# Kernel optimization log

Hardware: AMD Instinct MI355X
Metric: run time of the kernel (lower is better)

The kernel has to match this reference:

```python
import jax, jax.numpy as jnp
import numpy as np


def silu(x):
    return x * jax.nn.sigmoid(x)


def conv1x1(x, w, s, b, act):
    # x: [B,Ci,H,W], w: [Co,Ci]; BN folded into per-channel scale s / bias b
    y = jnp.einsum('oi,bihw->bohw', w, x) * s[None, :, None, None] + b[None, :, None, None]
    return silu(y) if act else y


def dwconv3x3(x, w, s, b):
    # depthwise 3x3, groups=C, padding SAME (autopad=1); w: [C,1,3,3]
    y = jax.lax.conv_general_dilated(
        x, w, window_strides=(1, 1), padding=[(1, 1), (1, 1)],
        dimension_numbers=('NCHW', 'OIHW', 'NCHW'),
        feature_group_count=x.shape[1])
    return y * s[None, :, None, None] + b[None, :, None, None]


def attention(x, qkv_w, qkv_s, qkv_b, pe_w, pe_s, pe_b, proj_w, proj_s, proj_b,
              num_heads=4, key_dim=32, head_dim=64):
    B, C, H, W = x.shape
    N = H * W
    scale = key_dim ** -0.5
    qkv = conv1x1(x, qkv_w, qkv_s, qkv_b, act=False)          # [B, C+2*nh*kd, H, W]
    qkv = qkv.reshape(B, num_heads, key_dim * 2 + head_dim, N)
    q = qkv[:, :, :key_dim]                                    # [B,nh,kd,N]
    k = qkv[:, :, key_dim:2 * key_dim]                         # [B,nh,kd,N]
    v = qkv[:, :, 2 * key_dim:]                                # [B,nh,hd,N]
    attn = jnp.einsum('bhdi,bhdj->bhij', q, k) * scale         # [B,nh,N,N]
    attn = jax.nn.softmax(attn, axis=-1)
    out = jnp.einsum('bhdj,bhij->bhdi', v, attn)               # [B,nh,hd,N]
    out = out.reshape(B, C, H, W) + dwconv3x3(v.reshape(B, C, H, W), pe_w, pe_s, pe_b)
    return conv1x1(out, proj_w, proj_s, proj_b, act=False)


def setup_inputs() -> dict:
    key = jax.random.key(0)
    ks = jax.random.split(key, 32)
    B, C1, H, W = 4, 512, 48, 48
    c = C1 // 2  # 256
    h = c + 2 * 32 * 4  # 512
    d = {'x': jax.random.normal(ks[0], (B, C1, H, W), jnp.float32)}
    def w(i, shape):
        return jax.random.normal(ks[i], shape, jnp.float32) * 0.05
    def s(i, n):
        return jax.random.uniform(ks[i], (n,), jnp.float32, 0.5, 1.5)
    def b(i, n):
        return jax.random.normal(ks[i], (n,), jnp.float32) * 0.05
    d['cv1_w'], d['cv1_s'], d['cv1_b'] = w(1, (2 * c, C1)), s(2, 2 * c), b(3, 2 * c)
    d['qkv_w'], d['qkv_s'], d['qkv_b'] = w(4, (h, c)), s(5, h), b(6, h)
    d['pe_w'], d['pe_s'], d['pe_b'] = w(7, (c, 1, 3, 3)), s(8, c), b(9, c)
    d['proj_w'], d['proj_s'], d['proj_b'] = w(10, (c, c)), s(11, c), b(12, c)
    d['ffn1_w'], d['ffn1_s'], d['ffn1_b'] = w(13, (2 * c, c)), s(14, 2 * c), b(15, 2 * c)
    d['ffn2_w'], d['ffn2_s'], d['ffn2_b'] = w(16, (c, 2 * c)), s(17, c), b(18, c)
    d['cv2_w'], d['cv2_s'], d['cv2_b'] = w(19, (C1, 2 * c)), s(20, C1), b(21, C1)
    return d


def reference(x, cv1_w, cv1_s, cv1_b, qkv_w, qkv_s, qkv_b, pe_w, pe_s, pe_b,
              proj_w, proj_s, proj_b, ffn1_w, ffn1_s, ffn1_b, ffn2_w, ffn2_s, ffn2_b,
              cv2_w, cv2_s, cv2_b):
    c = cv1_w.shape[0] // 2  # hidden channels (256)
    ab = conv1x1(x, cv1_w, cv1_s, cv1_b, act=True)
    a, bb = ab[:, :c], ab[:, c:]
    bb = bb + attention(bb, qkv_w, qkv_s, qkv_b, pe_w, pe_s, pe_b,
                        proj_w, proj_s, proj_b)
    f = conv1x1(bb, ffn1_w, ffn1_s, ffn1_b, act=True)
    bb = bb + conv1x1(f, ffn2_w, ffn2_s, ffn2_b, act=False)
    return conv1x1(jnp.concatenate([a, bb], axis=1), cv2_w, cv2_s, cv2_b, act=True)
```

## Files before the change

kernel.cpp:

```cpp
#include <hip/hip_runtime.h>
#include <math.h>

#define N_SP 2304
#define HW 48

typedef unsigned short u16;
typedef short s8v  __attribute__((ext_vector_type(8)));
typedef short s4v  __attribute__((ext_vector_type(4)));
typedef u16   u16x8 __attribute__((ext_vector_type(8)));
typedef float f32x4 __attribute__((ext_vector_type(4)));
typedef unsigned u32x4 __attribute__((ext_vector_type(4)));

__device__ __forceinline__ short f2bf(float x) {
    unsigned u = __float_as_uint(x);
    u += 0x7FFFu + ((u >> 16) & 1u);
    return (short)(u >> 16);
}
__device__ __forceinline__ float bf2f(u16 u) {
    return __uint_as_float((unsigned)u << 16);
}
__device__ __forceinline__ float fexp2(float x) { return __builtin_amdgcn_exp2f(x); }
__device__ __forceinline__ float frcp(float x)  { return __builtin_amdgcn_rcpf(x); }
__device__ __forceinline__ float fsilu(float v) {
    return v * frcp(1.f + fexp2(-1.4426950408889634f * v));
}
__device__ __forceinline__ unsigned cvtpk(float lo, float hi) {
    unsigned r;
    asm("v_cvt_pk_bf16_f32 %0, %1, %2" : "=v"(r) : "v"(lo), "v"(hi));
    return r;
}
__device__ __forceinline__ void gload16(const void* g, void* l) {
    __builtin_amdgcn_global_load_lds(
        (const __attribute__((address_space(1))) void*)g,
        (__attribute__((address_space(3))) void*)l, 16, 0, 0);
}
__device__ __forceinline__ void bar_lgkm() {
    asm volatile("s_waitcnt lgkmcnt(0)" ::: "memory");
    __builtin_amdgcn_s_barrier();
}

__global__ __launch_bounds__(256) void cvt_w(
    const float* __restrict__ s0, const float* __restrict__ s1,
    const float* __restrict__ s2, const float* __restrict__ s3,
    const float* __restrict__ s4, const float* __restrict__ s5,
    u16* __restrict__ d0, u16* __restrict__ d1, u16* __restrict__ d2,
    u16* __restrict__ d3, u16* __restrict__ d4, u16* __restrict__ d5)
{
    int id = blockIdx.x * 256 + threadIdx.x;
    const int c0 = 65536, c1 = c0 + 32768, c2 = c1 + 16384,
              c3 = c2 + 32768, c4 = c3 + 32768, c5 = c4 + 65536;
    if (id >= c5) return;
    const float* s; u16* d; int off;
    if      (id < c0) { s = s0; d = d0; off = id; }
    else if (id < c1) { s = s1; d = d1; off = id - c0; }
    else if (id < c2) { s = s2; d = d2; off = id - c1; }
    else if (id < c3) { s = s3; d = d3; off = id - c2; }
    else if (id < c4) { s = s4; d = d4; off = id - c3; }
    else              { s = s5; d = d5; off = id - c4; }
    float4 v = ((const float4*)s)[off];
    s4v p; p[0] = f2bf(v.x); p[1] = f2bf(v.y); p[2] = f2bf(v.z); p[3] = f2bf(v.w);
    ((s4v*)d)[off] = p;
}

__global__ __launch_bounds__(256) void transpose_x(const float* __restrict__ X,
                                                   u16* __restrict__ XT)
{
    __shared__ float tile[64][65];
    const int n0 = blockIdx.x * 64, c0 = blockIdx.y * 64, b = blockIdx.z;
    const float* src = X + (long)b * 512 * N_SP;
    u16* dst = XT + (long)b * N_SP * 512;
    const int t = threadIdx.x;
    #pragma unroll
    for (int it = 0; it < 16; ++it) {
        int id = t + 256 * it;
        int cl = id >> 6, nl = id & 63;
        tile[cl][nl] = src[(long)(c0 + cl) * N_SP + n0 + nl];
    }
    __syncthreads();
    #pragma unroll
    for (int it = 0; it < 16; ++it) {
        int id = t + 256 * it;
        int nl = id >> 6, cl = id & 63;
        dst[(long)(n0 + nl) * 512 + c0 + cl] = f2bf(tile[cl][nl]);
    }
}

template <int OMODE>
__global__ __launch_bounds__(256) void mfma_gemm(
    const u16* __restrict__ A1, const u16* __restrict__ A2, int K1,
    int sA1, int sA2, int K,
    const u16* __restrict__ W,
    const float* __restrict__ S, const float* __restrict__ Bi,
    const u16* __restrict__ Res, int sR,
    void* __restrict__ OutP, int sO, int Mtot,
    int act)
{
    __shared__ u16 Al[3][64][64];
    __shared__ u16 Bl[3][64][64];
    const int t  = threadIdx.x;
    const int n0 = blockIdx.x * 64;
    const int o0 = blockIdx.y * 64;
    const int lane = t & 63, w = t >> 6;
    const int wn = (w & 1) * 32, wo = (w >> 1) * 32;
    const int li = lane & 15, g = lane >> 4;

    const int b_blk = n0 / N_SP;
    const int n_in0 = n0 - b_blk * N_SP;

    f32x4 acc[2][2];
    #pragma unroll
    for (int fm = 0; fm < 2; ++fm)
        #pragma unroll
        for (int fn = 0; fn < 2; ++fn) acc[fm][fn] = f32x4{0.f, 0.f, 0.f, 0.f};

    auto issue = [&](int buf, int k0) {
        #pragma unroll
        for (int q = 0; q < 2; ++q) {
            int c = t + q * 256;
            int row = c >> 3;
            int col = ((c & 7) ^ (row & 7)) * 8;
            int kk = k0 + col;
            const u16* ga = (kk < K1) ? (A1 + (long)(n0 + row) * sA1 + kk)
                                      : (A2 + (long)(n0 + row) * sA2 + (kk - K1));
            gload16(ga, (u16*)Al[buf] + (q * 256 + w * 64) * 8);
            gload16(W + (long)(o0 + row) * K + k0 + col,
                    (u16*)Bl[buf] + (q * 256 + w * 64) * 8);
        }
    };

    const int NK = K >> 6;
    issue(0, 0);
    if (NK > 1) issue(1, 64);

    for (int ks = 0; ks < NK; ++ks) {
        if (ks + 1 < NK) asm volatile("s_waitcnt vmcnt(4)" ::: "memory");
        else             asm volatile("s_waitcnt vmcnt(0)" ::: "memory");
        __builtin_amdgcn_s_barrier();
        if (ks + 2 < NK) issue((ks + 2) % 3, (ks + 2) << 6);
        const int cur = ks % 3;
        #pragma unroll
        for (int k2 = 0; k2 < 2; ++k2) {
            s8v af[2], bfv[2];
            #pragma unroll
            for (int fm = 0; fm < 2; ++fm) {
                int row = wn + fm * 16 + li;
                af[fm] = *(const s8v*)&Al[cur][row][((g + 4 * k2) ^ (li & 7)) * 8];
            }
            #pragma unroll
            for (int fn = 0; fn < 2; ++fn) {
                int row = wo + fn * 16 + li;
                bfv[fn] = *(const s8v*)&Bl[cur][row][((g + 4 * k2) ^ (li & 7)) * 8];
            }
            #pragma unroll
            for (int fm = 0; fm < 2; ++fm)
                #pragma unroll
                for (int fn = 0; fn < 2; ++fn)
                    acc[fm][fn] = __builtin_amdgcn_mfma_f32_16x16x32_bf16(
                        af[fm], bfv[fn], acc[fm][fn], 0, 0, 0);
        }
    }

    #pragma unroll
    for (int fn = 0; fn < 2; ++fn) {
        const int o = o0 + wo + fn * 16 + li;
        const float sc2 = S[o], bi = Bi[o];
        #pragma unroll
        for (int fm = 0; fm < 2; ++fm) {
            const int nb  = n0 + wn + fm * 16 + 4 * g;
            const int nib = n_in0 + wn + fm * 16 + 4 * g;
            float y[4];
            #pragma unroll
            for (int r = 0; r < 4; ++r) {
                float v = acc[fm][fn][r] * sc2 + bi;
                if (act) v = fsilu(v);
                y[r] = v;
            }
            if (Res) {
                #pragma unroll
                for (int r = 0; r < 4; ++r)
                    y[r] += bf2f(Res[(long)(nb + r) * sR + o]);
            }
            if (OMODE == 0) {
                u16* O = (u16*)OutP;
                #pragma unroll
                for (int r = 0; r < 4; ++r)
                    O[(long)(nb + r) * sO + o] = (u16)f2bf(y[r]);
            } else if (OMODE == 1) {
                u16* O = (u16*)OutP + (long)b_blk * Mtot * N_SP + (long)o * N_SP + nib;
                s4v pk;
                #pragma unroll
                for (int r = 0; r < 4; ++r) pk[r] = f2bf(y[r]);
                *(s4v*)O = pk;
            } else {
                float* O = (float*)OutP + (long)b_blk * Mtot * N_SP + (long)o * N_SP + nib;
                *(float4*)O = make_float4(y[0], y[1], y[2], y[3]);
            }
        }
    }
}

__global__ __launch_bounds__(256) void attn_mfma(const u16* __restrict__ qkv,
    u16* __restrict__ Opart, float* __restrict__ mpart, float* __restrict__ lpart)
{
    const int N = N_SP;
    __shared__ u16 Klds[2][64][40];
    __shared__ u16 Vlds[2][64][72];

    const int i0 = blockIdx.x * 128;
    const int bh = blockIdx.y;
    const int z  = blockIdx.z;
    const int b = bh >> 2, h = bh & 3;
    const int t = threadIdx.x;
    const int w = t >> 6;
    const int lane = t & 63;
    const int li = lane & 15;
    const int g  = lane >> 4;
    const float qscale = 0.17677669529663687f * 1.4426950408889634f;

    const u16* qp = qkv + ((long)b * 512 + (long)h * 128) * N;
    const u16* kp = qp + 32L * N;
    const u16* vp = qp + 64L * N;

    const int ia = i0 + w * 16 + li;
    const int ib = ia + 64;

    s8v qf[2];
    #pragma unroll
    for (int r = 0; r < 8; ++r) {
        qf[0][r] = f2bf(bf2f(qp[(long)(8 * g + r) * N + ia]) * qscale);
        qf[1][r] = f2bf(bf2f(qp[(long)(8 * g + r) * N + ib]) * qscale);
    }

    f32x4 oacc[2][4];
    #pragma unroll
    for (int q = 0; q < 2; ++q)
        #pragma unroll
        for (int dt = 0; dt < 4; ++dt) oacc[q][dt] = f32x4{0.f, 0.f, 0.f, 0.f};
    float m_run[2] = {-1e30f, -1e30f}, l_run[2] = {0.f, 0.f};

    const int kj  = lane;
    const int kd0 = w * 8;
    const int vd  = t >> 2;
    const int vjb = (t & 3) * 16;

    const int jbase = z * 576;
    u16x8 kr, vr0, vr1;
    auto ldregs = [&](int j0) {
        const u16* kpp = kp + j0 + kj;
        #pragma unroll
        for (int u = 0; u < 8; ++u) kr[u] = kpp[(long)(kd0 + u) * N];
        vr0 = *(const u16x8*)(vp + (long)vd * N + j0 + vjb);
        vr1 = *(const u16x8*)(vp + (long)vd * N + j0 + vjb + 8);
    };

    ldregs(jbase);
    *(u16x8*)&Klds[0][kj][kd0]     = kr;
    *(u16x8*)&Vlds[0][vd][vjb]     = vr0;
    *(u16x8*)&Vlds[0][vd][vjb + 8] = vr1;
    ldregs(jbase + 64);
    bar_lgkm();

    int cur = 0;
    for (int it = 0; it < 9; ++it) {
        if (it + 1 < 9) {
            *(u16x8*)&Klds[cur ^ 1][kj][kd0]     = kr;
            *(u16x8*)&Vlds[cur ^ 1][vd][vjb]     = vr0;
            *(u16x8*)&Vlds[cur ^ 1][vd][vjb + 8] = vr1;
            if (it + 2 < 9) ldregs(jbase + (it + 2) * 64);
        }

        f32x4 sacc[2][4];
        #pragma unroll
        for (int js = 0; js < 4; ++js) {
            s8v kf = *(const s8v*)&Klds[cur][js * 16 + li][8 * g];
            f32x4 zz = f32x4{0.f, 0.f, 0.f, 0.f};
            sacc[0][js] = __builtin_amdgcn_mfma_f32_16x16x32_bf16(kf, qf[0], zz, 0, 0, 0);
            sacc[1][js] = __builtin_amdgcn_mfma_f32_16x16x32_bf16(kf, qf[1], zz, 0, 0, 0);
        }

        #pragma unroll
        for (int q = 0; q < 2; ++q) {
            float tm = -1e30f;
            #pragma unroll
            for (int js = 0; js < 4; ++js)
                #pragma unroll
                for (int r = 0; r < 4; ++r) tm = fmaxf(tm, sacc[q][js][r]);
            tm = fmaxf(tm, __shfl_xor(tm, 16, 64));
            tm = fmaxf(tm, __shfl_xor(tm, 32, 64));
            if (__any(tm > m_run[q] + 8.f)) {
                float mnew = fmaxf(m_run[q], tm);
                float scl  = fexp2(m_run[q] - mnew);
                l_run[q] *= scl;
                #pragma unroll
                for (int dt = 0; dt < 4; ++dt) oacc[q][dt] *= scl;
                m_run[q] = mnew;
            }
            float ts = 0.f;
            #pragma unroll
            for (int js = 0; js < 4; ++js)
                #pragma unroll
                for (int r = 0; r < 4; ++r) {
                    float p = fexp2(sacc[q][js][r] - m_run[q]);
                    sacc[q][js][r] = p;
                    ts += p;
                }
            ts += __shfl_xor(ts, 16, 64);
            ts += __shfl_xor(ts, 32, 64);
            l_run[q] += ts;
        }

        #pragma unroll
        for (int ks = 0; ks < 2; ++ks) {
            s8v pf[2];
            #pragma unroll
            for (int q = 0; q < 2; ++q) {
                u32x4 pw;
                pw[0] = cvtpk(sacc[q][2 * ks][0],     sacc[q][2 * ks][1]);
                pw[1] = cvtpk(sacc[q][2 * ks][2],     sacc[q][2 * ks][3]);
                pw[2] = cvtpk(sacc[q][2 * ks + 1][0], sacc[q][2 * ks + 1][1]);
                pw[3] = cvtpk(sacc[q][2 * ks + 1][2], sacc[q][2 * ks + 1][3]);
                pf[q] = __builtin_bit_cast(s8v, pw);
            }
            #pragma unroll
            for (int dt = 0; dt < 4; ++dt) {
                int d = dt * 16 + li;
                s4v lo = *(const s4v*)&Vlds[cur][d][32 * ks + 4 * g];
                s4v hi = *(const s4v*)&Vlds[cur][d][32 * ks + 16 + 4 * g];
                s8v vf = __builtin_shufflevector(lo, hi, 0, 1, 2, 3, 4, 5, 6, 7);
                oacc[0][dt] = __builtin_amdgcn_mfma_f32_16x16x32_bf16(vf, pf[0], oacc[0][dt], 0, 0, 0);
                oacc[1][dt] = __builtin_amdgcn_mfma_f32_16x16x32_bf16(vf, pf[1], oacc[1][dt], 0, 0, 0);
            }
        }

        if (it + 1 < 9) bar_lgkm();
        cur ^= 1;
    }

    const long cb = (long)(z * 16 + bh);
    #pragma unroll
    for (int q = 0; q < 2; ++q) {
        const int i = q ? ib : ia;
        #pragma unroll
        for (int dt = 0; dt < 4; ++dt)
            #pragma unroll
            for (int r = 0; r < 4; ++r)
                Opart[(cb * 64 + dt * 16 + 4 * g + r) * N + i] = (u16)f2bf(oacc[q][dt][r]);
        if (g == 0) {
            mpart[cb * N + i] = m_run[q];
            lpart[cb * N + i] = l_run[q];
        }
    }
}

__global__ __launch_bounds__(256) void attn_combine(
    const u16* __restrict__ Opart, const float* __restrict__ mpart,
    const float* __restrict__ lpart, const u16* __restrict__ qkv,
    const float* __restrict__ pw, const float* __restrict__ ps,
    const float* __restrict__ pb, u16* __restrict__ attnT)
{
    const int N = N_SP;
    const int i0 = blockIdx.x * 64;
    const int bh = blockIdx.y;
    const int b = bh >> 2, h = bh & 3;
    const int t = threadIdx.x;
    const int il = t & 63, dq = t >> 6;
    const int d0 = dq * 16;
    const int i = i0 + il;

    float mm[4], ll[4];
    #pragma unroll
    for (int c = 0; c < 4; ++c) {
        mm[c] = mpart[((long)(c * 16 + bh)) * N + i];
        ll[c] = lpart[((long)(c * 16 + bh)) * N + i];
    }
    float ms = fmaxf(fmaxf(mm[0], mm[1]), fmaxf(mm[2], mm[3]));
    float wc[4], lsum = 0.f;
    #pragma unroll
    for (int c = 0; c < 4; ++c) {
        wc[c] = fexp2(mm[c] - ms);
        lsum += wc[c] * ll[c];
    }
    float inv = frcp(lsum);

    const int y = i / HW, x = i - (i / HW) * HW;
    const int y0ok = (y > 0), y1ok = (y < HW - 1);
    const int x0ok = (x > 0), x1ok = (x < HW - 1);
    const u16* vbase = qkv + ((long)b * 512 + (long)h * 128 + 64) * N;

    u16 ob[16];
    #pragma unroll
    for (int dd = 0; dd < 16; ++dd) {
        const int d = d0 + dd;
        const int cg = h * 64 + d;
        float o = 0.f;
        #pragma unroll
        for (int c = 0; c < 4; ++c)
            o += wc[c] * bf2f(Opart[((long)(c * 16 + bh) * 64 + d) * N + i]);
        o *= inv;
        const u16* src = vbase + (long)d * N;
        const float* w9 = pw + cg * 9;
        float s = 0.f;
        #pragma unroll
        for (int dy = -1; dy <= 1; ++dy) {
            if ((dy < 0 && !y0ok) || (dy > 0 && !y1ok)) continue;
            const u16* row = src + (y + dy) * HW;
            if (x0ok) s += w9[(dy + 1) * 3 + 0] * bf2f(row[x - 1]);
            s += w9[(dy + 1) * 3 + 1] * bf2f(row[x]);
            if (x1ok) s += w9[(dy + 1) * 3 + 2] * bf2f(row[x + 1]);
        }
        o += s * ps[cg] + pb[cg];
        ob[dd] = (u16)f2bf(o);
    }
    u16* dst = attnT + ((long)b * N + i) * 256 + h * 64 + d0;
    *(u16x8*)dst       = *(u16x8*)&ob[0];
    *(u16x8*)(dst + 8) = *(u16x8*)&ob[8];
}

extern "C" void kernel_launch(void* const* d_in, const int* in_sizes, int n_in,
                              void* d_out, int out_size, void* d_ws, size_t ws_size,
                              hipStream_t stream)
{
    const long N = N_SP;
    const float* x      = (const float*)d_in[0];
    const float* cv1_w  = (const float*)d_in[1];
    const float* cv1_s  = (const float*)d_in[2];
    const float* cv1_b  = (const float*)d_in[3];
    const float* qkv_w  = (const float*)d_in[4];
    const float* qkv_s  = (const float*)d_in[5];
    const float* qkv_b  = (const float*)d_in[6];
    const float* pe_w   = (const float*)d_in[7];
    const float* pe_s   = (const float*)d_in[8];
    const float* pe_b   = (const float*)d_in[9];
    const float* proj_w = (const float*)d_in[10];
    const float* proj_s = (const float*)d_in[11];
    const float* proj_b = (const float*)d_in[12];
    const float* ffn1_w = (const float*)d_in[13];
    const float* ffn1_s = (const float*)d_in[14];
    const float* ffn1_b = (const float*)d_in[15];
    const float* ffn2_w = (const float*)d_in[16];
    const float* ffn2_s = (const float*)d_in[17];
    const float* ffn2_b = (const float*)d_in[18];
    const float* cv2_w  = (const float*)d_in[19];
    const float* cv2_s  = (const float*)d_in[20];
    const float* cv2_b  = (const float*)d_in[21];
    float* out = (float*)d_out;

    u16* ws = (u16*)d_ws;
    u16* xT      = ws;
    u16* abT     = xT      + 4L * N * 512;
    u16* qkvb    = abT     + 4L * N * 512;
    u16* attnT   = qkvb    + 4L * N * 512;
    u16* bb2T    = attnT   + 4L * N * 256;
    u16* fT      = bb2T    + 4L * N * 256;
    u16* bb3T    = fT      + 4L * N * 512;
    u16* w_cv1   = bb3T    + 4L * N * 256;
    u16* w_qkv   = w_cv1   + 512L * 512;
    u16* w_proj  = w_qkv   + 512L * 256;
    u16* w_ffn1  = w_proj  + 256L * 256;
    u16* w_ffn2  = w_ffn1  + 512L * 256;
    u16* w_cv2   = w_ffn2  + 256L * 512;
    u16* Opart   = w_cv2   + 512L * 512;
    float* mpart = (float*)(Opart + 4L * 16 * 64 * N);
    float* lpart = mpart + 4L * 16 * N;

    dim3 blk(256);
    const int BIGK = 1 << 28;

    cvt_w<<<960, blk, 0, stream>>>(cv1_w, qkv_w, proj_w, ffn1_w, ffn2_w, cv2_w,
                                   w_cv1, w_qkv, w_proj, w_ffn1, w_ffn2, w_cv2);
    transpose_x<<<dim3(36, 8, 4), blk, 0, stream>>>(x, xT);

    mfma_gemm<0><<<dim3(144, 8), blk, 0, stream>>>(
        xT, nullptr, BIGK, 512, 0, 512, w_cv1, cv1_s, cv1_b,
        nullptr, 0, abT, 512, 512, 1);

    mfma_gemm<1><<<dim3(144, 8), blk, 0, stream>>>(
        abT + 256, nullptr, BIGK, 512, 0, 256, w_qkv, qkv_s, qkv_b,
        nullptr, 0, qkvb, 0, 512, 0);

    attn_mfma<<<dim3(18, 16, 4), blk, 0, stream>>>(qkvb, Opart, mpart, lpart);

    attn_combine<<<dim3(36, 16), blk, 0, stream>>>(
        Opart, mpart, lpart, qkvb, pe_w, pe_s, pe_b, attnT);

    mfma_gemm<0><<<dim3(144, 4), blk, 0, stream>>>(
        attnT, nullptr, BIGK, 256, 0, 256, w_proj, proj_s, proj_b,
        abT + 256, 512, bb2T, 256, 256, 0);

    mfma_gemm<0><<<dim3(144, 8), blk, 0, stream>>>(
        bb2T, nullptr, BIGK, 256, 0, 256, w_ffn1, ffn1_s, ffn1_b,
        nullptr, 0, fT, 512, 512, 1);

    mfma_gemm<0><<<dim3(144, 4), blk, 0, stream>>>(
        fT, nullptr, BIGK, 512, 0, 512, w_ffn2, ffn2_s, ffn2_b,
        bb2T, 256, bb3T, 256, 256, 0);

    mfma_gemm<2><<<dim3(144, 8), blk, 0, stream>>>(
        abT, bb3T, 256, 512, 256, 512, w_cv2, cv2_s, cv2_b,
        nullptr, 0, out, 0, 512, 1);
}
```

Measured before the change: 148.8 us.

## Widen GEMM output tile to 128 with K-step 32 and halve attention KV splits

The GEMM kernel now computes 64x128 output tiles per block with a K step of 32 and a new 4-slot XOR swizzle, so each wave handles a 32x64 sub-tile with more MFMAs per A fragment load. The goal is more reuse of the activation tile per block and fewer blocks per GEMM. Separately, the split-K attention kernel drops from 4 to 2 key splits of 1152 keys each. That halves the Opart/mpart/lpart partial traffic and the combine work, but leaves half as many attention blocks to fill the GPU. Halving the block counts may hurt occupancy on a large CU count device.

Result: slower. 162.6 us (+9.3%).

```diff
diff --git a/kernel.cpp b/kernel.cpp
--- a/kernel.cpp
+++ b/kernel.cpp
@@ -95,73 +95,72 @@
     void* __restrict__ OutP, int sO, int Mtot,
     int act)
 {
-    __shared__ u16 Al[3][64][64];
-    __shared__ u16 Bl[3][64][64];
+    __shared__ u16 Al[3][64][32];
+    __shared__ u16 Bl[3][128][32];
     const int t  = threadIdx.x;
     const int n0 = blockIdx.x * 64;
-    const int o0 = blockIdx.y * 64;
+    const int o0 = blockIdx.y * 128;
     const int lane = t & 63, w = t >> 6;
-    const int wn = (w & 1) * 32, wo = (w >> 1) * 32;
+    const int wn = (w & 1) * 32, wo = (w >> 1) * 64;
     const int li = lane & 15, g = lane >> 4;
 
     const int b_blk = n0 / N_SP;
     const int n_in0 = n0 - b_blk * N_SP;
 
-    f32x4 acc[2][2];
+    f32x4 acc[2][4];
     #pragma unroll
     for (int fm = 0; fm < 2; ++fm)
         #pragma unroll
-        for (int fn = 0; fn < 2; ++fn) acc[fm][fn] = f32x4{0.f, 0.f, 0.f, 0.f};
+        for (int fn = 0; fn < 4; ++fn) acc[fm][fn] = f32x4{0.f, 0.f, 0.f, 0.f};
 
     auto issue = [&](int buf, int k0) {
-        #pragma unroll
-        for (int q = 0; q < 2; ++q) {
-            int c = t + q * 256;
-            int row = c >> 3;
-            int col = ((c & 7) ^ (row & 7)) * 8;
-            int kk = k0 + col;
+        {
+            int row = t >> 2, slot = t & 3;
+            int kk = k0 + ((slot ^ ((row >> 1) & 3)) << 3);
             const u16* ga = (kk < K1) ? (A1 + (long)(n0 + row) * sA1 + kk)
                                       : (A2 + (long)(n0 + row) * sA2 + (kk - K1));
-            gload16(ga, (u16*)Al[buf] + (q * 256 + w * 64) * 8);
-            gload16(W + (long)(o0 + row) * K + k0 + col,
-                    (u16*)Bl[buf] + (q * 256 + w * 64) * 8);
+            gload16(ga, (u16*)Al[buf] + t * 8);
+        }
+        #pragma unroll
+        for (int q = 0; q < 2; ++q) {
+            int idx = t + q * 256;
+            int row = idx >> 2, slot = idx & 3;
+            int kc = (slot ^ ((row >> 1) & 3)) << 3;
+            gload16(W + (long)(o0 + row) * K + k0 + kc, (u16*)Bl[buf] + idx * 8);
         }
     };
 
-    const int NK = K >> 6;
+    const int NK = K >> 5;
     issue(0, 0);
-    if (NK > 1) issue(1, 64);
+    if (NK > 1) issue(1, 32);
 
     for (int ks = 0; ks < NK; ++ks) {
-        if (ks + 1 < NK) asm volatile("s_waitcnt vmcnt(4)" ::: "memory");
+        if (ks + 1 < NK) asm volatile("s_waitcnt vmcnt(3)" ::: "memory");
         else             asm volatile("s_waitcnt vmcnt(0)" ::: "memory");
         __builtin_amdgcn_s_barrier();
-        if (ks + 2 < NK) issue((ks + 2) % 3, (ks + 2) << 6);
+        if (ks + 2 < NK) issue((ks + 2) % 3, (ks + 2) << 5);
         const int cur = ks % 3;
-        #pragma unroll
-        for (int k2 = 0; k2 < 2; ++k2) {
-            s8v af[2], bfv[2];
-            #pragma unroll
-            for (int fm = 0; fm < 2; ++fm) {
-                int row = wn + fm * 16 + li;
-                af[fm] = *(const s8v*)&Al[cur][row][((g + 4 * k2) ^ (li & 7)) * 8];
-            }
-            #pragma unroll
-            for (int fn = 0; fn < 2; ++fn) {
-                int row = wo + fn * 16 + li;
-                bfv[fn] = *(const s8v*)&Bl[cur][row][((g + 4 * k2) ^ (li & 7)) * 8];
-            }
-            #pragma unroll
-            for (int fm = 0; fm < 2; ++fm)
-                #pragma unroll
-                for (int fn = 0; fn < 2; ++fn)
-                    acc[fm][fn] = __builtin_amdgcn_mfma_f32_16x16x32_bf16(
-                        af[fm], bfv[fn], acc[fm][fn], 0, 0, 0);
-        }
-    }
-
-    #pragma unroll
-    for (int fn = 0; fn < 2; ++fn) {
+        s8v af[2], bfv[4];
+        #pragma unroll
+        for (int fm = 0; fm < 2; ++fm) {
+            int row = wn + fm * 16 + li;
+            af[fm] = *(const s8v*)&Al[cur][row][(g ^ ((row >> 1) & 3)) << 3];
+        }
+        #pragma unroll
+        for (int fn = 0; fn < 4; ++fn) {
+            int row = wo + fn * 16 + li;
+            bfv[fn] = *(const s8v*)&Bl[cur][row][(g ^ ((row >> 1) & 3)) << 3];
+        }
+        #pragma unroll
+        for (int fm = 0; fm < 2; ++fm)
+            #pragma unroll
+            for (int fn = 0; fn < 4; ++fn)
+                acc[fm][fn] = __builtin_amdgcn_mfma_f32_16x16x32_bf16(
+                    af[fm], bfv[fn], acc[fm][fn], 0, 0, 0);
+    }
+
+    #pragma unroll
+    for (int fn = 0; fn < 4; ++fn) {
         const int o = o0 + wo + fn * 16 + li;
         const float sc2 = S[o], bi = Bi[o];
         #pragma unroll
@@ -243,7 +242,8 @@
     const int vd  = t >> 2;
     const int vjb = (t & 3) * 16;
 
-    const int jbase = z * 576;
+    const int jbase = z * 1152;
+    const int NT = 18;
     u16x8 kr, vr0, vr1;
     auto ldregs = [&](int j0) {
         const u16* kpp = kp + j0 + kj;
@@ -261,12 +261,12 @@
     bar_lgkm();
 
     int cur = 0;
-    for (int it = 0; it < 9; ++it) {
-        if (it + 1 < 9) {
+    for (int it = 0; it < NT; ++it) {
+        if (it + 1 < NT) {
             *(u16x8*)&Klds[cur ^ 1][kj][kd0]     = kr;
             *(u16x8*)&Vlds[cur ^ 1][vd][vjb]     = vr0;
             *(u16x8*)&Vlds[cur ^ 1][vd][vjb + 8] = vr1;
-            if (it + 2 < 9) ldregs(jbase + (it + 2) * 64);
+            if (it + 2 < NT) ldregs(jbase + (it + 2) * 64);
         }
 
         f32x4 sacc[2][4];
@@ -332,7 +332,7 @@
             }
         }
 
-        if (it + 1 < 9) bar_lgkm();
+        if (it + 1 < NT) bar_lgkm();
         cur ^= 1;
     }
 
@@ -367,16 +367,16 @@
     const int d0 = dq * 16;
     const int i = i0 + il;
 
-    float mm[4], ll[4];
-    #pragma unroll
-    for (int c = 0; c < 4; ++c) {
+    float mm[2], ll[2];
+    #pragma unroll
+    for (int c = 0; c < 2; ++c) {
         mm[c] = mpart[((long)(c * 16 + bh)) * N + i];
         ll[c] = lpart[((long)(c * 16 + bh)) * N + i];
     }
-    float ms = fmaxf(fmaxf(mm[0], mm[1]), fmaxf(mm[2], mm[3]));
-    float wc[4], lsum = 0.f;
-    #pragma unroll
-    for (int c = 0; c < 4; ++c) {
+    float ms = fmaxf(mm[0], mm[1]);
+    float wc[2], lsum = 0.f;
+    #pragma unroll
+    for (int c = 0; c < 2; ++c) {
         wc[c] = fexp2(mm[c] - ms);
         lsum += wc[c] * ll[c];
     }
@@ -394,7 +394,7 @@
         const int cg = h * 64 + d;
         float o = 0.f;
         #pragma unroll
-        for (int c = 0; c < 4; ++c)
+        for (int c = 0; c < 2; ++c)
             o += wc[c] * bf2f(Opart[((long)(c * 16 + bh) * 64 + d) * N + i]);
         o *= inv;
         const u16* src = vbase + (long)d * N;
@@ -460,8 +460,8 @@
     u16* w_ffn2  = w_ffn1  + 512L * 256;
     u16* w_cv2   = w_ffn2  + 256L * 512;
     u16* Opart   = w_cv2   + 512L * 512;
-    float* mpart = (float*)(Opart + 4L * 16 * 64 * N);
-    float* lpart = mpart + 4L * 16 * N;
+    float* mpart = (float*)(Opart + 2L * 16 * 64 * N);
+    float* lpart = mpart + 2L * 16 * N;
 
     dim3 blk(256);
     const int BIGK = 1 << 28;
@@ -470,32 +470,32 @@
                                    w_cv1, w_qkv, w_proj, w_ffn1, w_ffn2, w_cv2);
     transpose_x<<<dim3(36, 8, 4), blk, 0, stream>>>(x, xT);
 
-    mfma_gemm<0><<<dim3(144, 8), blk, 0, stream>>>(
+    mfma_gemm<0><<<dim3(144, 4), blk, 0, stream>>>(
         xT, nullptr, BIGK, 512, 0, 512, w_cv1, cv1_s, cv1_b,
         nullptr, 0, abT, 512, 512, 1);
 
-    mfma_gemm<1><<<dim3(144, 8), blk, 0, stream>>>(
+    mfma_gemm<1><<<dim3(144, 4), blk, 0, stream>>>(
         abT + 256, nullptr, BIGK, 512, 0, 256, w_qkv, qkv_s, qkv_b,
         nullptr, 0, qkvb, 0, 512, 0);
 
-    attn_mfma<<<dim3(18, 16, 4), blk, 0, stream>>>(qkvb, Opart, mpart, lpart);
+    attn_mfma<<<dim3(18, 16, 2), blk, 0, stream>>>(qkvb, Opart, mpart, lpart);
 
     attn_combine<<<dim3(36, 16), blk, 0, stream>>>(
         Opart, mpart, lpart, qkvb, pe_w, pe_s, pe_b, attnT);
 
-    mfma_gemm<0><<<dim3(144, 4), blk, 0, stream>>>(
+    mfma_gemm<0><<<dim3(144, 2), blk, 0, stream>>>(
         attnT, nullptr, BIGK, 256, 0, 256, w_proj, proj_s, proj_b,
         abT + 256, 512, bb2T, 256, 256, 0);
 
-    mfma_gemm<0><<<dim3(144, 8), blk, 0, stream>>>(
+    mfma_gemm<0><<<dim3(144, 4), blk, 0, stream>>>(
         bb2T, nullptr, BIGK, 256, 0, 256, w_ffn1, ffn1_s, ffn1_b,
         nullptr, 0, fT, 512, 512, 1);
 
-    mfma_gemm<0><<<dim3(144, 4), blk, 0, stream>>>(
+    mfma_gemm<0><<<dim3(144, 2), blk, 0, stream>>>(
         fT, nullptr, BIGK, 512, 0, 512, w_ffn2, ffn2_s, ffn2_b,
         bb2T, 256, bb3T, 256, 256, 0);
 
-    mfma_gemm<2><<<dim3(144, 8), blk, 0, stream>>>(
+    mfma_gemm<2><<<dim3(144, 4), blk, 0, stream>>>(
         abT, bb3T, 256, 512, 256, 512, w_cv2, cv2_s, cv2_b,
         nullptr, 0, out, 0, 512, 1);
 }
```

## Remap block indices for XCD-local L2 reuse and merge prep kernels

Applied to the files above, without the earlier changes.

Flattens GEMM and attention grids to 1D and remaps block IDs so that blocks landing on the same XCD (block id mod 8) share the same spatial rows or batch-head slices. The aim is better L2 locality across the eight XCDs of the MI355X. It also fuses the weight conversion and input transpose kernels into one launch to save a kernel launch. The remap assumes round-robin XCD dispatch and grid sizes divisible by 8 and 18.

Measured after the change: 145.5 us. 1.02x faster.

```diff
diff --git a/kernel.cpp b/kernel.cpp
--- a/kernel.cpp
+++ b/kernel.cpp
@@ -39,37 +39,37 @@
     __builtin_amdgcn_s_barrier();
 }
 
-__global__ __launch_bounds__(256) void cvt_w(
+__global__ __launch_bounds__(256) void prep(
+    const float* __restrict__ X, u16* __restrict__ XT,
     const float* __restrict__ s0, const float* __restrict__ s1,
     const float* __restrict__ s2, const float* __restrict__ s3,
     const float* __restrict__ s4, const float* __restrict__ s5,
     u16* __restrict__ d0, u16* __restrict__ d1, u16* __restrict__ d2,
     u16* __restrict__ d3, u16* __restrict__ d4, u16* __restrict__ d5)
 {
-    int id = blockIdx.x * 256 + threadIdx.x;
-    const int c0 = 65536, c1 = c0 + 32768, c2 = c1 + 16384,
-              c3 = c2 + 32768, c4 = c3 + 32768, c5 = c4 + 65536;
-    if (id >= c5) return;
-    const float* s; u16* d; int off;
-    if      (id < c0) { s = s0; d = d0; off = id; }
-    else if (id < c1) { s = s1; d = d1; off = id - c0; }
-    else if (id < c2) { s = s2; d = d2; off = id - c1; }
-    else if (id < c3) { s = s3; d = d3; off = id - c2; }
-    else if (id < c4) { s = s4; d = d4; off = id - c3; }
-    else              { s = s5; d = d5; off = id - c4; }
-    float4 v = ((const float4*)s)[off];
-    s4v p; p[0] = f2bf(v.x); p[1] = f2bf(v.y); p[2] = f2bf(v.z); p[3] = f2bf(v.w);
-    ((s4v*)d)[off] = p;
-}
-
-__global__ __launch_bounds__(256) void transpose_x(const float* __restrict__ X,
-                                                   u16* __restrict__ XT)
-{
     __shared__ float tile[64][65];
-    const int n0 = blockIdx.x * 64, c0 = blockIdx.y * 64, b = blockIdx.z;
+    const int t = threadIdx.x;
+    if (blockIdx.x < 960) {
+        int id = blockIdx.x * 256 + t;
+        const int c0 = 65536, c1 = c0 + 32768, c2 = c1 + 16384,
+                  c3 = c2 + 32768, c4 = c3 + 32768, c5 = c4 + 65536;
+        if (id >= c5) return;
+        const float* s; u16* d; int off;
+        if      (id < c0) { s = s0; d = d0; off = id; }
+        else if (id < c1) { s = s1; d = d1; off = id - c0; }
+        else if (id < c2) { s = s2; d = d2; off = id - c1; }
+        else if (id < c3) { s = s3; d = d3; off = id - c2; }
+        else if (id < c4) { s = s4; d = d4; off = id - c3; }
+        else              { s = s5; d = d5; off = id - c4; }
+        float4 v = ((const float4*)s)[off];
+        s4v p; p[0] = f2bf(v.x); p[1] = f2bf(v.y); p[2] = f2bf(v.z); p[3] = f2bf(v.w);
+        ((s4v*)d)[off] = p;
+        return;
+    }
+    const int bid = blockIdx.x - 960;
+    const int n0 = (bid % 36) * 64, c0 = ((bid / 36) & 7) * 64, b = bid / 288;
     const float* src = X + (long)b * 512 * N_SP;
     u16* dst = XT + (long)b * N_SP * 512;
-    const int t = threadIdx.x;
     #pragma unroll
     for (int it = 0; it < 16; ++it) {
         int id = t + 256 * it;
@@ -85,7 +85,7 @@
     }
 }
 
-template <int OMODE>
+template <int NO, int OMODE>
 __global__ __launch_bounds__(256) void mfma_gemm(
     const u16* __restrict__ A1, const u16* __restrict__ A2, int K1,
     int sA1, int sA2, int K,
@@ -98,8 +98,10 @@
     __shared__ u16 Al[3][64][64];
     __shared__ u16 Bl[3][64][64];
     const int t  = threadIdx.x;
-    const int n0 = blockIdx.x * 64;
-    const int o0 = blockIdx.y * 64;
+    const int p = blockIdx.x;
+    const int cx = p & 7, q = p >> 3;
+    const int n0 = (cx * 18 + q / NO) * 64;
+    const int o0 = (q % NO) * 64;
     const int lane = t & 63, w = t >> 6;
     const int wn = (w & 1) * 32, wo = (w >> 1) * 32;
     const int li = lane & 15, g = lane >> 4;
@@ -115,16 +117,16 @@
 
     auto issue = [&](int buf, int k0) {
         #pragma unroll
-        for (int q = 0; q < 2; ++q) {
-            int c = t + q * 256;
+        for (int qq = 0; qq < 2; ++qq) {
+            int c = t + qq * 256;
             int row = c >> 3;
             int col = ((c & 7) ^ (row & 7)) * 8;
             int kk = k0 + col;
             const u16* ga = (kk < K1) ? (A1 + (long)(n0 + row) * sA1 + kk)
                                       : (A2 + (long)(n0 + row) * sA2 + (kk - K1));
-            gload16(ga, (u16*)Al[buf] + (q * 256 + w * 64) * 8);
+            gload16(ga, (u16*)Al[buf] + (qq * 256 + w * 64) * 8);
             gload16(W + (long)(o0 + row) * K + k0 + col,
-                    (u16*)Bl[buf] + (q * 256 + w * 64) * 8);
+                    (u16*)Bl[buf] + (qq * 256 + w * 64) * 8);
         }
     };
 
@@ -206,9 +208,11 @@
     __shared__ u16 Klds[2][64][40];
     __shared__ u16 Vlds[2][64][72];
 
-    const int i0 = blockIdx.x * 128;
-    const int bh = blockIdx.y;
-    const int z  = blockIdx.z;
+    const int p = blockIdx.x;
+    const int cx = p & 7, q = p >> 3;
+    const int i0 = (q % 18) * 128;
+    const int bhz = cx + 8 * (q / 18);
+    const int bh = bhz & 15, z = bhz >> 4;
     const int b = bh >> 2, h = bh & 3;
     const int t = threadIdx.x;
     const int w = t >> 6;
@@ -233,9 +237,9 @@
 
     f32x4 oacc[2][4];
     #pragma unroll
-    for (int q = 0; q < 2; ++q)
-        #pragma unroll
-        for (int dt = 0; dt < 4; ++dt) oacc[q][dt] = f32x4{0.f, 0.f, 0.f, 0.f};
+    for (int q2 = 0; q2 < 2; ++q2)
+        #pragma unroll
+        for (int dt = 0; dt < 4; ++dt) oacc[q2][dt] = f32x4{0.f, 0.f, 0.f, 0.f};
     float m_run[2] = {-1e30f, -1e30f}, l_run[2] = {0.f, 0.f};
 
     const int kj  = lane;
@@ -279,47 +283,47 @@
         }
 
         #pragma unroll
-        for (int q = 0; q < 2; ++q) {
+        for (int q2 = 0; q2 < 2; ++q2) {
             float tm = -1e30f;
             #pragma unroll
             for (int js = 0; js < 4; ++js)
                 #pragma unroll
-                for (int r = 0; r < 4; ++r) tm = fmaxf(tm, sacc[q][js][r]);
+                for (int r = 0; r < 4; ++r) tm = fmaxf(tm, sacc[q2][js][r]);
             tm = fmaxf(tm, __shfl_xor(tm, 16, 64));
             tm = fmaxf(tm, __shfl_xor(tm, 32, 64));
-            if (__any(tm > m_run[q] + 8.f)) {
-                float mnew = fmaxf(m_run[q], tm);
-                float scl  = fexp2(m_run[q] - mnew);
-                l_run[q] *= scl;
-                #pragma unroll
-                for (int dt = 0; dt < 4; ++dt) oacc[q][dt] *= scl;
-                m_run[q] = mnew;
+            if (__any(tm > m_run[q2] + 8.f)) {
+                float mnew = fmaxf(m_run[q2], tm);
+                float scl  = fexp2(m_run[q2] - mnew);
+                l_run[q2] *= scl;
+                #pragma unroll
+                for (int dt = 0; dt < 4; ++dt) oacc[q2][dt] *= scl;
+                m_run[q2] = mnew;
             }
             float ts = 0.f;
             #pragma unroll
             for (int js = 0; js < 4; ++js)
                 #pragma unroll
                 for (int r = 0; r < 4; ++r) {
-                    float p = fexp2(sacc[q][js][r] - m_run[q]);
-                    sacc[q][js][r] = p;
-                    ts += p;
+                    float pv = fexp2(sacc[q2][js][r] - m_run[q2]);
+                    sacc[q2][js][r] = pv;
+                    ts += pv;
                 }
             ts += __shfl_xor(ts, 16, 64);
             ts += __shfl_xor(ts, 32, 64);
-            l_run[q] += ts;
+            l_run[q2] += ts;
         }
 
         #pragma unroll
         for (int ks = 0; ks < 2; ++ks) {
             s8v pf[2];
             #pragma unroll
-            for (int q = 0; q < 2; ++q) {
+            for (int q2 = 0; q2 < 2; ++q2) {
                 u32x4 pw;
-                pw[0] = cvtpk(sacc[q][2 * ks][0],     sacc[q][2 * ks][1]);
-                pw[1] = cvtpk(sacc[q][2 * ks][2],     sacc[q][2 * ks][3]);
-                pw[2] = cvtpk(sacc[q][2 * ks + 1][0], sacc[q][2 * ks + 1][1]);
-                pw[3] = cvtpk(sacc[q][2 * ks + 1][2], sacc[q][2 * ks + 1][3]);
-                pf[q] = __builtin_bit_cast(s8v, pw);
+                pw[0] = cvtpk(sacc[q2][2 * ks][0],     sacc[q2][2 * ks][1]);
+                pw[1] = cvtpk(sacc[q2][2 * ks][2],     sacc[q2][2 * ks][3]);
+                pw[2] = cvtpk(sacc[q2][2 * ks + 1][0], sacc[q2][2 * ks + 1][1]);
+                pw[3] = cvtpk(sacc[q2][2 * ks + 1][2], sacc[q2][2 * ks + 1][3]);
+                pf[q2] = __builtin_bit_cast(s8v, pw);
             }
             #pragma unroll
             for (int dt = 0; dt < 4; ++dt) {
@@ -338,16 +342,16 @@
 
     const long cb = (long)(z * 16 + bh);
     #pragma unroll
-    for (int q = 0; q < 2; ++q) {
-        const int i = q ? ib : ia;
+    for (int q2 = 0; q2 < 2; ++q2) {
+        const int i = q2 ? ib : ia;
         #pragma unroll
         for (int dt = 0; dt < 4; ++dt)
             #pragma unroll
             for (int r = 0; r < 4; ++r)
-                Opart[(cb * 64 + dt * 16 + 4 * g + r) * N + i] = (u16)f2bf(oacc[q][dt][r]);
+                Opart[(cb * 64 + dt * 16 + 4 * g + r) * N + i] = (u16)f2bf(oacc[q2][dt][r]);
         if (g == 0) {
-            mpart[cb * N + i] = m_run[q];
-            lpart[cb * N + i] = l_run[q];
+            mpart[cb * N + i] = m_run[q2];
+            lpart[cb * N + i] = l_run[q2];
         }
     }
 }
@@ -466,36 +470,36 @@
     dim3 blk(256);
     const int BIGK = 1 << 28;
 
-    cvt_w<<<960, blk, 0, stream>>>(cv1_w, qkv_w, proj_w, ffn1_w, ffn2_w, cv2_w,
-                                   w_cv1, w_qkv, w_proj, w_ffn1, w_ffn2, w_cv2);
-    transpose_x<<<dim3(36, 8, 4), blk, 0, stream>>>(x, xT);
-
-    mfma_gemm<0><<<dim3(144, 8), blk, 0, stream>>>(
+    prep<<<2112, blk, 0, stream>>>(x, xT,
+        cv1_w, qkv_w, proj_w, ffn1_w, ffn2_w, cv2_w,
+        w_cv1, w_qkv, w_proj, w_ffn1, w_ffn2, w_cv2);
+
+    mfma_gemm<8, 0><<<1152, blk, 0, stream>>>(
         xT, nullptr, BIGK, 512, 0, 512, w_cv1, cv1_s, cv1_b,
         nullptr, 0, abT, 512, 512, 1);
 
-    mfma_gemm<1><<<dim3(144, 8), blk, 0, stream>>>(
+    mfma_gemm<8, 1><<<1152, blk, 0, stream>>>(
         abT + 256, nullptr, BIGK, 512, 0, 256, w_qkv, qkv_s, qkv_b,
         nullptr, 0, qkvb, 0, 512, 0);
 
-    attn_mfma<<<dim3(18, 16, 4), blk, 0, stream>>>(qkvb, Opart, mpart, lpart);
+    attn_mfma<<<1152, blk, 0, stream>>>(qkvb, Opart, mpart, lpart);
 
     attn_combine<<<dim3(36, 16), blk, 0, stream>>>(
         Opart, mpart, lpart, qkvb, pe_w, pe_s, pe_b, attnT);
 
-    mfma_gemm<0><<<dim3(144, 4), blk, 0, stream>>>(
+    mfma_gemm<4, 0><<<576, blk, 0, stream>>>(
         attnT, nullptr, BIGK, 256, 0, 256, w_proj, proj_s, proj_b,
         abT + 256, 512, bb2T, 256, 256, 0);
 
-    mfma_gemm<0><<<dim3(144, 8), blk, 0, stream>>>(
+    mfma_gemm<8, 0><<<1152, blk, 0, stream>>>(
         bb2T, nullptr, BIGK, 256, 0, 256, w_ffn1, ffn1_s, ffn1_b,
         nullptr, 0, fT, 512, 512, 1);
 
-    mfma_gemm<0><<<dim3(144, 4), blk, 0, stream>>>(
+    mfma_gemm<4, 0><<<576, blk, 0, stream>>>(
         fT, nullptr, BIGK, 512, 0, 512, w_ffn2, ffn2_s, ffn2_b,
         bb2T, 256, bb3T, 256, 256, 0);
 
-    mfma_gemm<2><<<dim3(144, 8), blk, 0, stream>>>(
+    mfma_gemm<8, 2><<<1152, blk, 0, stream>>>(
         abT, bb3T, 256, 512, 256, 512, w_cv2, cv2_s, cv2_b,
         nullptr, 0, out, 0, 512, 1);
 }
```
